# Kernel tuning notes

Measured on AMD Instinct MI355X. Metric: run time of the kernel, lower is better.

Reference implementation:

```python
import jax, jax.numpy as jnp
import numpy as np

HIDDEN = 512
ANN = 512


def setup_inputs() -> dict:
    key = jax.random.key(0)
    k1, k2, k3, k4, k5, k6 = jax.random.split(key, 6)
    B, S = 32, 4096
    prev_hidden_state = jax.random.normal(k1, (B, HIDDEN), dtype=jnp.float32)
    annotations = jax.random.normal(k2, (B, S, ANN), dtype=jnp.float32)
    in_dim = HIDDEN + ANN
    # Kaiming-uniform-ish init like torch Linear
    lim1 = 1.0 / np.sqrt(in_dim)
    W1 = jax.random.uniform(k3, (in_dim, HIDDEN), dtype=jnp.float32, minval=-lim1, maxval=lim1)
    b1 = jax.random.uniform(k4, (HIDDEN,), dtype=jnp.float32, minval=-lim1, maxval=lim1)
    lim2 = 1.0 / np.sqrt(HIDDEN)
    W2 = jax.random.uniform(k5, (HIDDEN, 1), dtype=jnp.float32, minval=-lim2, maxval=lim2)
    b2 = jax.random.uniform(k6, (1,), dtype=jnp.float32, minval=-lim2, maxval=lim2)
    return {"prev_hidden_state": prev_hidden_state, "annotations": annotations,
            "W1": W1, "b1": b1, "W2": W2, "b2": b2}


def reference(prev_hidden_state, annotations, W1, b1, W2, b2):
    # Split W1 so we never materialize the [B,S,hidden+ann] concat:
    # concat([h_rep, ann]) @ W1 == h @ W1[:H] + ann @ W1[H:]
    W1_h, W1_a = W1[:HIDDEN], W1[HIDDEN:]
    # [B,1,H] + [B,S,H] -> [B,S,H]
    pre = prev_hidden_state @ W1_h  # [B,H]
    hidden = jnp.tanh(pre[:, None, :] + jnp.einsum('bsa,ah->bsh', annotations, W1_a) + b1)
    score = jnp.einsum('bsh,h->bs', hidden, W2[:, 0]) + b2[0]  # [B,S]
    alpha = jax.nn.softmax(score, axis=1)  # legacy F.softmax default dim=1
    # alpha.bmm(annotations): [B,1,S] @ [B,S,A] -> [B,1,A]
    context = jnp.einsum('bs,bsa->ba', alpha, annotations)[:, None, :]
    return context
```

## Files before the change

### kernel.cpp

```cpp
#include <hip/hip_runtime.h>

#define HID 512
#define SEQ 4096
#define NB 32
#define BS 64
#define NCHUNK (SEQ / BS)
#define CH_STRIDE 514

typedef __attribute__((ext_vector_type(8))) __bf16 bf16x8;
typedef __attribute__((ext_vector_type(16))) float f32x16;

__device__ __forceinline__ float tanh_fast(float v) {
    float e = __expf(2.f * v);
    return 1.f - __fdividef(2.f, e + 1.f);
}

__global__ void build_w1af(const float* __restrict__ W1,
                           unsigned short* __restrict__ w1af) {
    __shared__ float tile[64][65];
    int t = threadIdx.x;
    int lane = t & 63;
    int r4 = t >> 6;
    int k0 = blockIdx.x * 64;
    int h0 = blockIdx.y * 64;
#pragma unroll
    for (int i = 0; i < 16; ++i) {
        int r = i * 4 + r4;
        tile[r][lane] = W1[(size_t)(HID + k0 + r) * HID + h0 + lane];
    }
    __syncthreads();
#pragma unroll
    for (int i = 0; i < 16; ++i) {
        int hr = i * 4 + r4;
        int h = h0 + hr, k = k0 + lane;
        __bf16 bv = (__bf16)tile[lane][hr];
        int ht = h >> 5, hl = h & 31;
        int ks = k >> 4, g = (k >> 3) & 1, j = k & 7;
        size_t off = (((size_t)ht * 32 + ks) * 64 + g * 32 + hl) * 8 + j;
        w1af[off] = *(unsigned short*)&bv;
    }
}

__global__ void pre_partial(const float* __restrict__ prev,
                            const float* __restrict__ W1,
                            float* __restrict__ pre_part) {
    __shared__ float pl[128];
    int kc = blockIdx.x;
    int b  = blockIdx.y;
    int t  = threadIdx.x;
    if (t < 128) pl[t] = prev[b * HID + kc * 128 + t];
    __syncthreads();
    int h0 = 2 * t;
    float ax = 0.f, ay = 0.f;
    for (int k = 0; k < 128; ++k) {
        float pv = pl[k];
        float2 wv = *(const float2*)(W1 + (size_t)(kc * 128 + k) * HID + h0);
        ax += pv * wv.x;
        ay += pv * wv.y;
    }
    float* dst = pre_part + ((size_t)b * 4 + kc) * HID + h0;
    dst[0] = ax; dst[1] = ay;
}

__global__ __launch_bounds__(512, 4)
void score_ctx(const float* __restrict__ ann,
               const unsigned short* __restrict__ w1af,
               const float* __restrict__ pre_part,
               const float* __restrict__ b1,
               const float* __restrict__ W2,
               float* __restrict__ cout) {
    __shared__ unsigned short ann_lds[BS * 512];
    __shared__ float pre_lds[512];
    __shared__ float w2_lds[512];
    __shared__ float red[8][64];
    __shared__ float p_lds[64];
    __shared__ float md[2];

    int chunk = blockIdx.x;
    int b = blockIdx.y;
    int s0 = chunk * BS;
    int t = threadIdx.x;
    int w = t >> 6;
    int lane = t & 63;
    int sl = lane & 31;
    int g  = lane >> 5;

    {
        float pp = b1[t];
#pragma unroll
        for (int kc = 0; kc < 4; ++kc)
            pp += pre_part[((size_t)b * 4 + kc) * HID + t];
        pre_lds[t] = pp;
        w2_lds[t] = W2[t];
    }

    const float* abase = ann + ((size_t)b * SEQ + s0) * 512;
#pragma unroll
    for (int i = 0; i < 8; ++i) {
        int c = t + i * 512;
        int row = c >> 6;
        int k8 = (c & 63) << 3;
        const float4* src = (const float4*)(abase + (size_t)row * 512 + k8);
        float4 f0 = src[0], f1 = src[1];
        bf16x8 pk;
        pk[0] = (__bf16)f0.x; pk[1] = (__bf16)f0.y;
        pk[2] = (__bf16)f0.z; pk[3] = (__bf16)f0.w;
        pk[4] = (__bf16)f1.x; pk[5] = (__bf16)f1.y;
        pk[6] = (__bf16)f1.z; pk[7] = (__bf16)f1.w;
        unsigned boff = ((unsigned)(row * 512 + k8) * 2u) ^ ((unsigned)(row & 7) << 4);
        *(bf16x8*)((char*)ann_lds + boff) = pk;
    }
    __syncthreads();

    int h0 = w * 64;
    const unsigned short* wb0 = w1af + (size_t)(2 * w) * 16384 + (size_t)lane * 8;
    const unsigned short* wb1 = wb0 + 16384;
    unsigned be0 = ((unsigned)(sl * 512 + g * 8)) * 2u;
    unsigned be1 = ((unsigned)((32 + sl) * 512 + g * 8)) * 2u;
    unsigned swz = (unsigned)(sl & 7) << 4;

    f32x16 acc00, acc01, acc10, acc11;
#pragma unroll
    for (int r = 0; r < 16; ++r) { acc00[r] = 0.f; acc01[r] = 0.f; acc10[r] = 0.f; acc11[r] = 0.f; }

    bf16x8 pa0 = *(const bf16x8*)(wb0);
    bf16x8 pa1 = *(const bf16x8*)(wb1);
    bf16x8 na0, na1;

#pragma unroll 1
    for (int c = 0; c < 16; ++c) {
        {
            int kn = 2 * c + 1;
            na0 = *(const bf16x8*)(wb0 + kn * 512);
            na1 = *(const bf16x8*)(wb1 + kn * 512);
            unsigned kb = (unsigned)(2 * c) * 32u;
            bf16x8 b0 = *(const bf16x8*)((const char*)ann_lds + ((be0 + kb) ^ swz));
            bf16x8 b1f = *(const bf16x8*)((const char*)ann_lds + ((be1 + kb) ^ swz));
            acc00 = __builtin_amdgcn_mfma_f32_32x32x16_bf16(pa0, b0, acc00, 0, 0, 0);
            acc01 = __builtin_amdgcn_mfma_f32_32x32x16_bf16(pa0, b1f, acc01, 0, 0, 0);
            acc10 = __builtin_amdgcn_mfma_f32_32x32x16_bf16(pa1, b0, acc10, 0, 0, 0);
            acc11 = __builtin_amdgcn_mfma_f32_32x32x16_bf16(pa1, b1f, acc11, 0, 0, 0);
        }
        {
            int kn = (c < 15) ? (2 * c + 2) : 0;
            pa0 = *(const bf16x8*)(wb0 + kn * 512);
            pa1 = *(const bf16x8*)(wb1 + kn * 512);
            unsigned kb = (unsigned)(2 * c + 1) * 32u;
            bf16x8 b0 = *(const bf16x8*)((const char*)ann_lds + ((be0 + kb) ^ swz));
            bf16x8 b1f = *(const bf16x8*)((const char*)ann_lds + ((be1 + kb) ^ swz));
            acc00 = __builtin_amdgcn_mfma_f32_32x32x16_bf16(na0, b0, acc00, 0, 0, 0);
            acc01 = __builtin_amdgcn_mfma_f32_32x32x16_bf16(na0, b1f, acc01, 0, 0, 0);
            acc10 = __builtin_amdgcn_mfma_f32_32x32x16_bf16(na1, b0, acc10, 0, 0, 0);
            acc11 = __builtin_amdgcn_mfma_f32_32x32x16_bf16(na1, b1f, acc11, 0, 0, 0);
        }
    }

    float sp0 = 0.f, sp1 = 0.f;
#pragma unroll
    for (int r = 0; r < 16; ++r) {
        int hl = (r & 3) + 8 * (r >> 2) + 4 * g;
        float pra = pre_lds[h0 + hl],      w2a = w2_lds[h0 + hl];
        float prb = pre_lds[h0 + 32 + hl], w2b = w2_lds[h0 + 32 + hl];
        sp0 += w2a * tanh_fast(acc00[r] + pra) + w2b * tanh_fast(acc10[r] + prb);
        sp1 += w2a * tanh_fast(acc01[r] + pra) + w2b * tanh_fast(acc11[r] + prb);
    }
    sp0 += __shfl_xor(sp0, 32);
    sp1 += __shfl_xor(sp1, 32);
    if (lane < 32) {
        red[w][lane]      = sp0;
        red[w][32 + lane] = sp1;
    }
    __syncthreads();

    if (w == 0) {
        float sc = 0.f;
#pragma unroll
        for (int wv = 0; wv < 8; ++wv) sc += red[wv][lane];
        float m = sc;
#pragma unroll
        for (int off = 32; off; off >>= 1) m = fmaxf(m, __shfl_xor(m, off));
        float p = __expf(sc - m);
        float d = p;
#pragma unroll
        for (int off = 32; off; off >>= 1) d += __shfl_xor(d, off);
        p_lds[lane] = p;
        if (lane == 0) { md[0] = m; md[1] = d; }
    }
    __syncthreads();

    float na = 0.f;
#pragma unroll 8
    for (int s = 0; s < BS; ++s) {
        float pv = p_lds[s];
        unsigned boff = ((unsigned)(s * 512 + t) * 2u) ^ ((unsigned)(s & 7) << 4);
        unsigned short us = *(const unsigned short*)((const char*)ann_lds + boff);
        float av = __uint_as_float((unsigned)us << 16);
        na += pv * av;
    }
    float* cb = cout + (size_t)(b * NCHUNK + chunk) * CH_STRIDE;
    cb[2 + t] = na;
    if (t == 0) { cb[0] = md[0]; cb[1] = md[1]; }
}

__global__ void finalize_ctx(const float* __restrict__ cout,
                             float* __restrict__ out) {
    __shared__ float scale[NCHUNK];
    __shared__ float stats[2];
    int b = blockIdx.x;
    int t = threadIdx.x;
    if (t < 64) {
        const float* cb = cout + (size_t)(b * NCHUNK + t) * CH_STRIDE;
        float m = cb[0], d = cb[1];
        float M = m;
#pragma unroll
        for (int off = 32; off; off >>= 1) M = fmaxf(M, __shfl_xor(M, off));
        float sc = __expf(m - M);
        scale[t] = sc;
        float dd = sc * d;
#pragma unroll
        for (int off = 32; off; off >>= 1) dd += __shfl_xor(dd, off);
        if (t == 0) { stats[0] = M; stats[1] = dd; }
    }
    __syncthreads();
    float inv = 1.f / stats[1];
    int a0 = 2 * t;
    float ax = 0.f, ay = 0.f;
    for (int c = 0; c < NCHUNK; ++c) {
        float sc = scale[c];
        const float2 nv = *(const float2*)(cout + (size_t)(b * NCHUNK + c) * CH_STRIDE + 2 + a0);
        ax += sc * nv.x;
        ay += sc * nv.y;
    }
    out[(size_t)b * 512 + a0]     = ax * inv;
    out[(size_t)b * 512 + a0 + 1] = ay * inv;
}

extern "C" void kernel_launch(void* const* d_in, const int* in_sizes, int n_in,
                              void* d_out, int out_size, void* d_ws, size_t ws_size,
                              hipStream_t stream) {
    (void)in_sizes; (void)n_in; (void)out_size; (void)ws_size;
    const float* prev = (const float*)d_in[0];
    const float* ann  = (const float*)d_in[1];
    const float* W1   = (const float*)d_in[2];
    const float* b1   = (const float*)d_in[3];
    const float* W2   = (const float*)d_in[4];
    float* out = (float*)d_out;

    char* ws = (char*)d_ws;
    unsigned short* w1af = (unsigned short*)ws;
    float* pre_part = (float*)(ws + 524288);
    float* cout     = (float*)(ws + 524288 + 262144);

    build_w1af<<<dim3(8, 8), dim3(256), 0, stream>>>(W1, w1af);
    pre_partial<<<dim3(4, NB), dim3(256), 0, stream>>>(prev, W1, pre_part);
    score_ctx<<<dim3(NCHUNK, NB), dim3(512), 0, stream>>>(ann, w1af, pre_part, b1, W2, cout);
    finalize_ctx<<<dim3(NB), dim3(256), 0, stream>>>(cout, out);
}
```

Measured before the change: 143.7 us.

## Loop over multiple chunks per block with double-buffered LDS and online softmax

Each block of 1024 threads now processes eight 64-row chunks of annotations and prefetches the next chunk into registers while computing the current one. It keeps a running max/denominator and context accumulator (online softmax), so only eight partials per batch go to finalize. The intent is to overlap global loads with MFMA work and cut the partial write/reduce traffic. In exchange, the grid shrinks to 256 large blocks with 128 KB of LDS each, and every chunk adds extra barriers, which may reduce latency hiding.

```diff
diff --git a/kernel.cpp b/kernel.cpp
--- a/kernel.cpp
+++ b/kernel.cpp
@@ -4,8 +4,9 @@
 #define SEQ 4096
 #define NB 32
 #define BS 64
-#define NCHUNK (SEQ / BS)
-#define CH_STRIDE 514
+#define NSB 8
+#define CPB 8
+#define CH2 1026
 
 typedef __attribute__((ext_vector_type(8))) __bf16 bf16x8;
 typedef __attribute__((ext_vector_type(16))) float f32x16;
@@ -62,177 +63,186 @@
     dst[0] = ax; dst[1] = ay;
 }
 
-__global__ __launch_bounds__(512, 4)
+__global__ __launch_bounds__(1024, 4)
 void score_ctx(const float* __restrict__ ann,
                const unsigned short* __restrict__ w1af,
                const float* __restrict__ pre_part,
                const float* __restrict__ b1,
                const float* __restrict__ W2,
                float* __restrict__ cout) {
-    __shared__ unsigned short ann_lds[BS * 512];
+    __shared__ unsigned short annA[BS * 512];
+    __shared__ unsigned short annB[BS * 512];
     __shared__ float pre_lds[512];
     __shared__ float w2_lds[512];
-    __shared__ float red[8][64];
+    __shared__ float red[16][64];
     __shared__ float p_lds[64];
     __shared__ float md[2];
 
-    int chunk = blockIdx.x;
-    int b = blockIdx.y;
-    int s0 = chunk * BS;
-    int t = threadIdx.x;
-    int w = t >> 6;
-    int lane = t & 63;
-    int sl = lane & 31;
-    int g  = lane >> 5;
-
-    {
+    const int sb = blockIdx.x, b = blockIdx.y;
+    const int t = threadIdx.x;
+    const int wv = t >> 6;
+    const int lane = t & 63;
+    const int sl = lane & 31;
+    const int g = lane >> 5;
+
+    if (t < 512) {
         float pp = b1[t];
 #pragma unroll
         for (int kc = 0; kc < 4; ++kc)
             pp += pre_part[((size_t)b * 4 + kc) * HID + t];
         pre_lds[t] = pp;
-        w2_lds[t] = W2[t];
-    }
-
-    const float* abase = ann + ((size_t)b * SEQ + s0) * 512;
-#pragma unroll
-    for (int i = 0; i < 8; ++i) {
-        int c = t + i * 512;
-        int row = c >> 6;
-        int k8 = (c & 63) << 3;
-        const float4* src = (const float4*)(abase + (size_t)row * 512 + k8);
-        float4 f0 = src[0], f1 = src[1];
-        bf16x8 pk;
-        pk[0] = (__bf16)f0.x; pk[1] = (__bf16)f0.y;
-        pk[2] = (__bf16)f0.z; pk[3] = (__bf16)f0.w;
-        pk[4] = (__bf16)f1.x; pk[5] = (__bf16)f1.y;
-        pk[6] = (__bf16)f1.z; pk[7] = (__bf16)f1.w;
-        unsigned boff = ((unsigned)(row * 512 + k8) * 2u) ^ ((unsigned)(row & 7) << 4);
-        *(bf16x8*)((char*)ann_lds + boff) = pk;
+    } else {
+        w2_lds[t - 512] = W2[t - 512];
+    }
+
+    const float* abase = ann + ((size_t)b * SEQ + (size_t)sb * (CPB * BS)) * 512;
+
+    float4 sf[8];
+    {
+#pragma unroll
+        for (int i = 0; i < 4; ++i) {
+            int idx = t + i * 1024;
+            const float4* src = (const float4*)(abase + (size_t)(idx >> 6) * 512 + (idx & 63) * 8);
+            sf[2 * i] = src[0]; sf[2 * i + 1] = src[1];
+        }
+#pragma unroll
+        for (int i = 0; i < 4; ++i) {
+            int idx = t + i * 1024;
+            int row = idx >> 6, k8 = (idx & 63) * 8;
+            bf16x8 pk;
+            pk[0] = (__bf16)sf[2*i].x;   pk[1] = (__bf16)sf[2*i].y;
+            pk[2] = (__bf16)sf[2*i].z;   pk[3] = (__bf16)sf[2*i].w;
+            pk[4] = (__bf16)sf[2*i+1].x; pk[5] = (__bf16)sf[2*i+1].y;
+            pk[6] = (__bf16)sf[2*i+1].z; pk[7] = (__bf16)sf[2*i+1].w;
+            unsigned boff = ((unsigned)(row * 512 + k8) * 2u) ^ ((unsigned)(row & 7) << 4);
+            *(bf16x8*)((char*)annA + boff) = pk;
+        }
     }
     __syncthreads();
 
-    int h0 = w * 64;
-    const unsigned short* wb0 = w1af + (size_t)(2 * w) * 16384 + (size_t)lane * 8;
-    const unsigned short* wb1 = wb0 + 16384;
-    unsigned be0 = ((unsigned)(sl * 512 + g * 8)) * 2u;
-    unsigned be1 = ((unsigned)((32 + sl) * 512 + g * 8)) * 2u;
-    unsigned swz = (unsigned)(sl & 7) << 4;
-
-    f32x16 acc00, acc01, acc10, acc11;
-#pragma unroll
-    for (int r = 0; r < 16; ++r) { acc00[r] = 0.f; acc01[r] = 0.f; acc10[r] = 0.f; acc11[r] = 0.f; }
-
-    bf16x8 pa0 = *(const bf16x8*)(wb0);
-    bf16x8 pa1 = *(const bf16x8*)(wb1);
-    bf16x8 na0, na1;
+    float m_run = -3.0e38f, d_run = 0.f, ctx = 0.f;
+    const int col = t & 511, half = t >> 9;
+
+    const unsigned short* wb = w1af + (size_t)wv * 16384 + (size_t)lane * 8;
+    const unsigned be0 = (unsigned)(sl * 512 + g * 8) * 2u;
+    const unsigned be1 = (unsigned)((32 + sl) * 512 + g * 8) * 2u;
+    const unsigned swz = (unsigned)(sl & 7) << 4;
 
 #pragma unroll 1
-    for (int c = 0; c < 16; ++c) {
-        {
-            int kn = 2 * c + 1;
-            na0 = *(const bf16x8*)(wb0 + kn * 512);
-            na1 = *(const bf16x8*)(wb1 + kn * 512);
-            unsigned kb = (unsigned)(2 * c) * 32u;
-            bf16x8 b0 = *(const bf16x8*)((const char*)ann_lds + ((be0 + kb) ^ swz));
-            bf16x8 b1f = *(const bf16x8*)((const char*)ann_lds + ((be1 + kb) ^ swz));
-            acc00 = __builtin_amdgcn_mfma_f32_32x32x16_bf16(pa0, b0, acc00, 0, 0, 0);
-            acc01 = __builtin_amdgcn_mfma_f32_32x32x16_bf16(pa0, b1f, acc01, 0, 0, 0);
-            acc10 = __builtin_amdgcn_mfma_f32_32x32x16_bf16(pa1, b0, acc10, 0, 0, 0);
-            acc11 = __builtin_amdgcn_mfma_f32_32x32x16_bf16(pa1, b1f, acc11, 0, 0, 0);
-        }
-        {
-            int kn = (c < 15) ? (2 * c + 2) : 0;
-            pa0 = *(const bf16x8*)(wb0 + kn * 512);
-            pa1 = *(const bf16x8*)(wb1 + kn * 512);
-            unsigned kb = (unsigned)(2 * c + 1) * 32u;
-            bf16x8 b0 = *(const bf16x8*)((const char*)ann_lds + ((be0 + kb) ^ swz));
-            bf16x8 b1f = *(const bf16x8*)((const char*)ann_lds + ((be1 + kb) ^ swz));
-            acc00 = __builtin_amdgcn_mfma_f32_32x32x16_bf16(na0, b0, acc00, 0, 0, 0);
-            acc01 = __builtin_amdgcn_mfma_f32_32x32x16_bf16(na0, b1f, acc01, 0, 0, 0);
-            acc10 = __builtin_amdgcn_mfma_f32_32x32x16_bf16(na1, b0, acc10, 0, 0, 0);
-            acc11 = __builtin_amdgcn_mfma_f32_32x32x16_bf16(na1, b1f, acc11, 0, 0, 0);
-        }
-    }
-
-    float sp0 = 0.f, sp1 = 0.f;
-#pragma unroll
-    for (int r = 0; r < 16; ++r) {
-        int hl = (r & 3) + 8 * (r >> 2) + 4 * g;
-        float pra = pre_lds[h0 + hl],      w2a = w2_lds[h0 + hl];
-        float prb = pre_lds[h0 + 32 + hl], w2b = w2_lds[h0 + 32 + hl];
-        sp0 += w2a * tanh_fast(acc00[r] + pra) + w2b * tanh_fast(acc10[r] + prb);
-        sp1 += w2a * tanh_fast(acc01[r] + pra) + w2b * tanh_fast(acc11[r] + prb);
-    }
-    sp0 += __shfl_xor(sp0, 32);
-    sp1 += __shfl_xor(sp1, 32);
-    if (lane < 32) {
-        red[w][lane]      = sp0;
-        red[w][32 + lane] = sp1;
-    }
-    __syncthreads();
-
-    if (w == 0) {
-        float sc = 0.f;
-#pragma unroll
-        for (int wv = 0; wv < 8; ++wv) sc += red[wv][lane];
-        float m = sc;
-#pragma unroll
-        for (int off = 32; off; off >>= 1) m = fmaxf(m, __shfl_xor(m, off));
-        float p = __expf(sc - m);
-        float d = p;
-#pragma unroll
-        for (int off = 32; off; off >>= 1) d += __shfl_xor(d, off);
-        p_lds[lane] = p;
-        if (lane == 0) { md[0] = m; md[1] = d; }
-    }
-    __syncthreads();
-
-    float na = 0.f;
+    for (int c = 0; c < CPB; ++c) {
+        unsigned short* curb = (c & 1) ? annB : annA;
+        unsigned short* nxtb = (c & 1) ? annA : annB;
+
+        if (c < CPB - 1) {
+            const float* ab = abase + (size_t)(c + 1) * BS * 512;
+#pragma unroll
+            for (int i = 0; i < 4; ++i) {
+                int idx = t + i * 1024;
+                const float4* src = (const float4*)(ab + (size_t)(idx >> 6) * 512 + (idx & 63) * 8);
+                sf[2 * i] = src[0]; sf[2 * i + 1] = src[1];
+            }
+        }
+
+        f32x16 acc0, acc1;
+#pragma unroll
+        for (int r = 0; r < 16; ++r) { acc0[r] = 0.f; acc1[r] = 0.f; }
+#pragma unroll 2
+        for (int ks = 0; ks < 32; ++ks) {
+            bf16x8 a = *(const bf16x8*)(wb + ks * 512);
+            bf16x8 bf0 = *(const bf16x8*)((const char*)curb + ((be0 + (unsigned)ks * 32u) ^ swz));
+            bf16x8 bf1 = *(const bf16x8*)((const char*)curb + ((be1 + (unsigned)ks * 32u) ^ swz));
+            acc0 = __builtin_amdgcn_mfma_f32_32x32x16_bf16(a, bf0, acc0, 0, 0, 0);
+            acc1 = __builtin_amdgcn_mfma_f32_32x32x16_bf16(a, bf1, acc1, 0, 0, 0);
+        }
+
+        float sp0 = 0.f, sp1 = 0.f;
+#pragma unroll
+        for (int r = 0; r < 16; ++r) {
+            int h = wv * 32 + (r & 3) + 8 * (r >> 2) + 4 * g;
+            float pr = pre_lds[h], w2v = w2_lds[h];
+            sp0 += w2v * tanh_fast(acc0[r] + pr);
+            sp1 += w2v * tanh_fast(acc1[r] + pr);
+        }
+        sp0 += __shfl_xor(sp0, 32);
+        sp1 += __shfl_xor(sp1, 32);
+        if (lane < 32) { red[wv][lane] = sp0; red[wv][32 + lane] = sp1; }
+        __syncthreads();
+
+        if (wv == 0) {
+            float sc = 0.f;
+#pragma unroll
+            for (int q = 0; q < 16; ++q) sc += red[q][lane];
+            float m = sc;
+#pragma unroll
+            for (int off = 32; off; off >>= 1) m = fmaxf(m, __shfl_xor(m, off));
+            float p = __expf(sc - m);
+            float d = p;
+#pragma unroll
+            for (int off = 32; off; off >>= 1) d += __shfl_xor(d, off);
+            p_lds[lane] = p;
+            if (lane == 0) { md[0] = m; md[1] = d; }
+        }
+        __syncthreads();
+
+        float m_c = md[0], d_c = md[1];
+        float m_new = fmaxf(m_run, m_c);
+        float sc_old = __expf(m_run - m_new);
+        float sc_c = __expf(m_c - m_new);
+        d_run = d_run * sc_old + d_c * sc_c;
+        float na = 0.f;
+        const char* cb8 = (const char*)curb;
 #pragma unroll 8
-    for (int s = 0; s < BS; ++s) {
-        float pv = p_lds[s];
-        unsigned boff = ((unsigned)(s * 512 + t) * 2u) ^ ((unsigned)(s & 7) << 4);
-        unsigned short us = *(const unsigned short*)((const char*)ann_lds + boff);
-        float av = __uint_as_float((unsigned)us << 16);
-        na += pv * av;
-    }
-    float* cb = cout + (size_t)(b * NCHUNK + chunk) * CH_STRIDE;
-    cb[2 + t] = na;
-    if (t == 0) { cb[0] = md[0]; cb[1] = md[1]; }
+        for (int s2 = 0; s2 < 32; ++s2) {
+            int s = half * 32 + s2;
+            unsigned boff = ((unsigned)(s * 512 + col) * 2u) ^ ((unsigned)(s & 7) << 4);
+            unsigned short us = *(const unsigned short*)(cb8 + boff);
+            na += p_lds[s] * __uint_as_float((unsigned)us << 16);
+        }
+        ctx = ctx * sc_old + na * sc_c;
+        m_run = m_new;
+
+        if (c < CPB - 1) {
+            __syncthreads();
+#pragma unroll
+            for (int i = 0; i < 4; ++i) {
+                int idx = t + i * 1024;
+                int row = idx >> 6, k8 = (idx & 63) * 8;
+                bf16x8 pk;
+                pk[0] = (__bf16)sf[2*i].x;   pk[1] = (__bf16)sf[2*i].y;
+                pk[2] = (__bf16)sf[2*i].z;   pk[3] = (__bf16)sf[2*i].w;
+                pk[4] = (__bf16)sf[2*i+1].x; pk[5] = (__bf16)sf[2*i+1].y;
+                pk[6] = (__bf16)sf[2*i+1].z; pk[7] = (__bf16)sf[2*i+1].w;
+                unsigned boff = ((unsigned)(row * 512 + k8) * 2u) ^ ((unsigned)(row & 7) << 4);
+                *(bf16x8*)((char*)nxtb + boff) = pk;
+            }
+            __syncthreads();
+        }
+    }
+
+    float* cb = cout + ((size_t)b * NSB + sb) * CH2;
+    cb[2 + half * 512 + col] = ctx;
+    if (t == 0) { cb[0] = m_run; cb[1] = d_run; }
 }
 
 __global__ void finalize_ctx(const float* __restrict__ cout,
                              float* __restrict__ out) {
-    __shared__ float scale[NCHUNK];
-    __shared__ float stats[2];
-    int b = blockIdx.x;
-    int t = threadIdx.x;
-    if (t < 64) {
-        const float* cb = cout + (size_t)(b * NCHUNK + t) * CH_STRIDE;
-        float m = cb[0], d = cb[1];
-        float M = m;
-#pragma unroll
-        for (int off = 32; off; off >>= 1) M = fmaxf(M, __shfl_xor(M, off));
-        float sc = __expf(m - M);
-        scale[t] = sc;
-        float dd = sc * d;
-#pragma unroll
-        for (int off = 32; off; off >>= 1) dd += __shfl_xor(dd, off);
-        if (t == 0) { stats[0] = M; stats[1] = dd; }
-    }
-    __syncthreads();
-    float inv = 1.f / stats[1];
-    int a0 = 2 * t;
-    float ax = 0.f, ay = 0.f;
-    for (int c = 0; c < NCHUNK; ++c) {
-        float sc = scale[c];
-        const float2 nv = *(const float2*)(cout + (size_t)(b * NCHUNK + c) * CH_STRIDE + 2 + a0);
-        ax += sc * nv.x;
-        ay += sc * nv.y;
-    }
-    out[(size_t)b * 512 + a0]     = ax * inv;
-    out[(size_t)b * 512 + a0 + 1] = ay * inv;
+    int b = blockIdx.x, t = threadIdx.x;
+    float ms[NSB];
+    float M = -3.0e38f;
+#pragma unroll
+    for (int s = 0; s < NSB; ++s) {
+        ms[s] = cout[((size_t)b * NSB + s) * CH2];
+        M = fmaxf(M, ms[s]);
+    }
+    float D = 0.f, val = 0.f;
+#pragma unroll
+    for (int s = 0; s < NSB; ++s) {
+        const float* cb = cout + ((size_t)b * NSB + s) * CH2;
+        float e = __expf(ms[s] - M);
+        D += e * cb[1];
+        val += e * (cb[2 + t] + cb[2 + 512 + t]);
+    }
+    out[(size_t)b * 512 + t] = val / D;
 }
 
 extern "C" void kernel_launch(void* const* d_in, const int* in_sizes, int n_in,
@@ -253,6 +263,6 @@
 
     build_w1af<<<dim3(8, 8), dim3(256), 0, stream>>>(W1, w1af);
     pre_partial<<<dim3(4, NB), dim3(256), 0, stream>>>(prev, W1, pre_part);
-    score_ctx<<<dim3(NCHUNK, NB), dim3(512), 0, stream>>>(ann, w1af, pre_part, b1, W2, cout);
-    finalize_ctx<<<dim3(NB), dim3(256), 0, stream>>>(cout, out);
-}
+    score_ctx<<<dim3(NSB, NB), dim3(1024), 0, stream>>>(ann, w1af, pre_part, b1, W2, cout);
+    finalize_ctx<<<dim3(NB), dim3(512), 0, stream>>>(cout, out);
+}
```

After: 151.6 us. 1.06x slower.
